# Kernel tuning notes

Hardware: AMD Instinct MI355X
Metric: run time of the kernel (lower is better)

## Reference

```python
import jax, jax.numpy as jnp
import numpy as np

GN_EPS = 1e-5
G = 8          # SKA groups
SKS3 = 27      # sks**3


def _aff(x, s, b):
    # folded BatchNorm (eval): per-channel scale + shift on NCDHW tensor
    return x * s[None, :, None, None, None] + b[None, :, None, None, None]


def _c1(x, w):
    # 1x1x1 conv as channel GEMM; w: [O, I]
    return jnp.einsum('bcdhw,oc->bodhw', x, w)


def _dw5(x, w):
    # depthwise 5x5x5 conv, pad=2; w: [C, 1, 5, 5, 5]
    return jax.lax.conv_general_dilated(
        x, w, window_strides=(1, 1, 1), padding=[(2, 2)] * 3,
        dimension_numbers=('NCDHW', 'OIDHW', 'NCDHW'),
        feature_group_count=x.shape[1])


def setup_inputs() -> dict:
    key = jax.random.key(0)
    ks = jax.random.split(key, 24)
    B, C, D, H, W = 2, 64, 32, 32, 32

    def n(k, shape, scale=1.0):
        return jax.random.normal(k, shape, jnp.float32) * scale

    def u(k, shape):
        return jax.random.uniform(k, shape, jnp.float32, 0.5, 1.5)

    return {
        'x': n(ks[0], (B, C, D, H, W)),
        'w1': n(ks[1], (32, 64), 64 ** -0.5),
        's1': u(ks[2], (32,)), 'b1': n(ks[3], (32,), 0.1),
        'w2': n(ks[4], (32, 1, 5, 5, 5), 125 ** -0.5),
        's2': u(ks[5], (32,)), 'b2': n(ks[6], (32,), 0.1),
        'w3': n(ks[7], (32, 32), 32 ** -0.5),
        's3': u(ks[8], (32,)), 'b3': n(ks[9], (32,), 0.1),
        'w4': n(ks[10], (216, 32), 32 ** -0.5), 'b4': n(ks[11], (216,), 0.1),
        'gn_g': u(ks[12], (216,)), 'gn_b': n(ks[13], (216,), 0.1),
        'bn_s': u(ks[14], (64,)), 'bn_b': n(ks[15], (64,), 0.1),
        'pw1_w': n(ks[16], (128, 64), 64 ** -0.5),
        'pw1_s': u(ks[17], (128,)), 'pw1_b': n(ks[18], (128,), 0.1),
        'pw2_w': n(ks[19], (64, 128), 128 ** -0.5),
        'pw2_s': u(ks[20], (64,)), 'pw2_b': n(ks[21], (64,), 0.1),
    }


def reference(x, w1, s1, b1, w2, s2, b2, w3, s3, b3, w4, b4,
              gn_g, gn_b, bn_s, bn_b,
              pw1_w, pw1_s, pw1_b, pw2_w, pw2_s, pw2_b):
    B, C, D, H, W = x.shape

    # ---- LKP3D: dynamic kernel generation ----
    a = jax.nn.relu(_aff(_c1(x, w1), s1, b1))          # cv1 + BN + ReLU
    a = _aff(_dw5(a, w2), s2, b2)                      # cv2 (5^3 dw) + BN
    a = jax.nn.relu(_aff(_c1(a, w3), s3, b3))          # cv3 + BN + ReLU
    wk = _c1(a, w4) + b4[None, :, None, None, None]    # cv4: [B,216,D,H,W]
    # GroupNorm: num_groups = dim//groups = 8, channels = 216
    g = wk.reshape(B, G, SKS3, D, H, W)
    mu = g.mean(axis=(2, 3, 4, 5), keepdims=True)
    var = g.var(axis=(2, 3, 4, 5), keepdims=True)
    g = (g - mu) * jax.lax.rsqrt(var + GN_EPS)
    wk = g.reshape(B, G * SKS3, D, H, W) * gn_g[None, :, None, None, None] \
         + gn_b[None, :, None, None, None]
    wk = wk.reshape(B, G, SKS3, D, H, W)               # [B, G, 27, D, H, W]

    # ---- SKA3D: apply dynamic kernels (27 shifted copies, grouped) ----
    offs = [(di, hi, wi) for di in (-1, 0, 1) for hi in (-1, 0, 1) for wi in (-1, 0, 1)]
    patches = jnp.stack(
        [jnp.roll(x, (-di, -hi, -wi), axis=(2, 3, 4)) for di, hi, wi in offs],
        axis=2)                                        # [B, C, 27, D, H, W]
    p = patches.reshape(B, G, C // G, SKS3, D, H, W)
    sk = jnp.einsum('bgckdhw,bgkdhw->bgcdhw', p, wk).reshape(B, C, D, H, W)

    y = _aff(sk, bn_s, bn_b) + x                       # LSConv BN + residual

    # ---- FFN (residual): pw1 + BN + ReLU + pw2 + BN ----
    f = jax.nn.relu(_aff(_c1(y, pw1_w), pw1_s, pw1_b))
    f = _aff(_c1(f, pw2_w), pw2_s, pw2_b)
    return y + f
```

## Files before the change

### kernel.cpp

```cpp
#include <hip/hip_runtime.h>
#include <hip/hip_bf16.h>

#define SPAT 32768
#define BATCH 2
#define GN_EPS 1e-5f

__device__ __forceinline__ void fma4(float4& a, const float4& v, float w) {
    a.x = fmaf(v.x, w, a.x); a.y = fmaf(v.y, w, a.y);
    a.z = fmaf(v.z, w, a.z); a.w = fmaf(v.w, w, a.w);
}

template <bool RELU, bool AFF>
__global__ __launch_bounds__(256) void k_c1(
    const float* __restrict__ in, const float* __restrict__ w,
    const float* __restrict__ sc, const float* __restrict__ bi,
    float* __restrict__ out, int Cin, int Cout)
{
    int q = blockIdx.x * 256 + threadIdx.x;
    int s = q * 4;
    int o0 = blockIdx.y * 4, b = blockIdx.z;
    const float* ip = in + (size_t)b * Cin * SPAT + s;
    float4 a0 = {0,0,0,0}, a1 = a0, a2 = a0, a3 = a0;
#pragma unroll 4
    for (int c = 0; c < Cin; ++c) {
        float4 v = *(const float4*)(ip + (size_t)c * SPAT);
        fma4(a0, v, w[(o0+0)*Cin + c]);
        fma4(a1, v, w[(o0+1)*Cin + c]);
        fma4(a2, v, w[(o0+2)*Cin + c]);
        fma4(a3, v, w[(o0+3)*Cin + c]);
    }
    float4 accs[4] = {a0, a1, a2, a3};
#pragma unroll
    for (int i = 0; i < 4; ++i) {
        int o = o0 + i;
        float scale = AFF ? sc[o] : 1.f;
        float shift = bi[o];
        float4 r = accs[i];
        r.x = r.x * scale + shift; r.y = r.y * scale + shift;
        r.z = r.z * scale + shift; r.w = r.w * scale + shift;
        if (RELU) {
            r.x = fmaxf(r.x, 0.f); r.y = fmaxf(r.y, 0.f);
            r.z = fmaxf(r.z, 0.f); r.w = fmaxf(r.w, 0.f);
        }
        *(float4*)(out + ((size_t)b * Cout + o) * SPAT + s) = r;
    }
}

__global__ __launch_bounds__(256) void k_dw5(
    const float* __restrict__ in, const float* __restrict__ w2,
    const float* __restrict__ s2, const float* __restrict__ b2,
    float* __restrict__ out)
{
    __shared__ float lds[8 * 36 * 40];
    int tid = threadIdx.x;
    int d0 = blockIdx.x * 4;
    int c = blockIdx.y, b = blockIdx.z;
    const float* ip = in + ((size_t)(b * 32 + c)) * SPAT;

    float4 z = {0,0,0,0};
    for (int i = tid; i < 8 * 36 * 40 / 4; i += 256)
        ((float4*)lds)[i] = z;
    __syncthreads();
    for (int i = tid; i < 8 * 256; i += 256) {
        int p = i >> 8, rem = i & 255;
        int r = rem >> 3, c4 = (rem & 7) * 4;
        int d = d0 - 2 + p;
        if (d >= 0 && d < 32) {
            float4 v = *(const float4*)(ip + d * 1024 + r * 32 + c4);
            *(float4*)&lds[p * 1440 + (r + 2) * 40 + (c4 + 4)] = v;
        }
    }
    __syncthreads();

    float scl = s2[c], shf = b2[c];
    const float* wt = w2 + c * 125;
#pragma unroll
    for (int k = 0; k < 4; ++k) {
        int j = tid + k * 256;
        int pd = j >> 8, rem = j & 255;
        int hr = rem >> 3, w4 = (rem & 7) * 4;
        float4 acc = {0,0,0,0};
#pragma unroll
        for (int kd = 0; kd < 5; ++kd) {
            const float* pl = &lds[(pd + kd) * 1440];
#pragma unroll
            for (int kh = 0; kh < 5; ++kh) {
                const float* row = pl + (hr + kh) * 40 + w4;
                float4 r0 = *(const float4*)(row);
                float4 r1 = *(const float4*)(row + 4);
                float4 r2 = *(const float4*)(row + 8);
                float win[12] = {r0.x, r0.y, r0.z, r0.w,
                                 r1.x, r1.y, r1.z, r1.w,
                                 r2.x, r2.y, r2.z, r2.w};
#pragma unroll
                for (int kw = 0; kw < 5; ++kw) {
                    float wv = wt[kd * 25 + kh * 5 + kw];
                    acc.x = fmaf(wv, win[2 + 0 + kw], acc.x);
                    acc.y = fmaf(wv, win[2 + 1 + kw], acc.y);
                    acc.z = fmaf(wv, win[2 + 2 + kw], acc.z);
                    acc.w = fmaf(wv, win[2 + 3 + kw], acc.w);
                }
            }
        }
        acc.x = acc.x * scl + shf; acc.y = acc.y * scl + shf;
        acc.z = acc.z * scl + shf; acc.w = acc.w * scl + shf;
        *(float4*)(out + ((size_t)(b * 32 + c)) * SPAT
                   + (d0 + pd) * 1024 + hr * 32 + w4) = acc;
    }
}

__global__ __launch_bounds__(256) void k_gn_part(
    const float* __restrict__ wk, float* __restrict__ partial)
{
    int bg = blockIdx.y;
    const float4* p = (const float4*)(wk + (size_t)bg * 27 * SPAT
                                      + (size_t)blockIdx.x * 16384);
    float sum = 0.f, ss = 0.f;
    for (int i = threadIdx.x; i < 4096; i += 256) {
        float4 v = p[i];
        sum += v.x + v.y + v.z + v.w;
        ss += v.x*v.x + v.y*v.y + v.z*v.z + v.w*v.w;
    }
    __shared__ float sh[512];
    sh[threadIdx.x] = sum; sh[256 + threadIdx.x] = ss;
    __syncthreads();
    for (int off = 128; off > 0; off >>= 1) {
        if (threadIdx.x < off) {
            sh[threadIdx.x] += sh[threadIdx.x + off];
            sh[256 + threadIdx.x] += sh[256 + threadIdx.x + off];
        }
        __syncthreads();
    }
    if (threadIdx.x == 0) {
        partial[(bg * 54 + blockIdx.x) * 2 + 0] = sh[0];
        partial[(bg * 54 + blockIdx.x) * 2 + 1] = sh[256];
    }
}

__global__ void k_gn_final(const float* __restrict__ partial, float* __restrict__ stats)
{
    int bg = blockIdx.x;
    int t = threadIdx.x;
    float sum = 0.f, ss = 0.f;
    if (t < 54) {
        sum = partial[(bg * 54 + t) * 2 + 0];
        ss  = partial[(bg * 54 + t) * 2 + 1];
    }
#pragma unroll
    for (int off = 32; off > 0; off >>= 1) {
        sum += __shfl_down(sum, off, 64);
        ss  += __shfl_down(ss,  off, 64);
    }
    if (t == 0) {
        stats[bg * 2 + 0] = sum;
        stats[bg * 2 + 1] = ss;
    }
}

__global__ __launch_bounds__(256) void k_ska(
    const float* __restrict__ x, const float* __restrict__ wk,
    const float* __restrict__ stats,
    const float* __restrict__ gn_g, const float* __restrict__ gn_b,
    const float* __restrict__ bn_s, const float* __restrict__ bn_b,
    float* __restrict__ y)
{
    int q = blockIdx.x * 256 + threadIdx.x;
    int s = q * 4;
    int g = blockIdx.y, b = blockIdx.z;
    int bg = b * 8 + g;
    const float N = 27.f * (float)SPAT;
    float mu  = stats[bg * 2 + 0] / N;
    float var = stats[bg * 2 + 1] / N - mu * mu;
    float inv = rsqrtf(var + GN_EPS);
    int d = s >> 10, h = (s >> 5) & 31, w0 = s & 31;
    const float* xg = x + ((size_t)(b * 64 + g * 8)) * SPAT;
    const float* wp = wk + ((size_t)(b * 216 + g * 27)) * SPAT + s;

    float4 acc[8];
#pragma unroll
    for (int c = 0; c < 8; ++c) acc[c] = {0,0,0,0};

#pragma unroll
    for (int kd = 0; kd < 3; ++kd) {
        int zd = (d + kd + 31) & 31;
#pragma unroll
        for (int kh = 0; kh < 3; ++kh) {
            int zh = (h + kh + 31) & 31;
            int kbase = (kd * 3 + kh) * 3;
            float wn[3][4];
#pragma unroll
            for (int kw = 0; kw < 3; ++kw) {
                int kk = kbase + kw;
                float4 wq = *(const float4*)(wp + (size_t)kk * SPAT);
                float gg = gn_g[g * 27 + kk], gb = gn_b[g * 27 + kk];
                wn[kw][0] = (wq.x - mu) * inv * gg + gb;
                wn[kw][1] = (wq.y - mu) * inv * gg + gb;
                wn[kw][2] = (wq.z - mu) * inv * gg + gb;
                wn[kw][3] = (wq.w - mu) * inv * gg + gb;
            }
            int rowoff = zd * 1024 + zh * 32;
#pragma unroll
            for (int c = 0; c < 8; ++c) {
                const float* row = xg + (size_t)c * SPAT + rowoff;
                float4 m = *(const float4*)(row + w0);
                float xl = row[(w0 + 31) & 31];
                float xr = row[(w0 + 4) & 31];
                float win[6] = {xl, m.x, m.y, m.z, m.w, xr};
#pragma unroll
                for (int kw = 0; kw < 3; ++kw) {
                    acc[c].x = fmaf(win[0 + kw], wn[kw][0], acc[c].x);
                    acc[c].y = fmaf(win[1 + kw], wn[kw][1], acc[c].y);
                    acc[c].z = fmaf(win[2 + kw], wn[kw][2], acc[c].z);
                    acc[c].w = fmaf(win[3 + kw], wn[kw][3], acc[c].w);
                }
            }
        }
    }
#pragma unroll
    for (int c = 0; c < 8; ++c) {
        int ch = g * 8 + c;
        float4 xc = *(const float4*)(xg + (size_t)c * SPAT + s);
        float bs = bn_s[ch], bb = bn_b[ch];
        float4 r;
        r.x = acc[c].x * bs + bb + xc.x;
        r.y = acc[c].y * bs + bb + xc.y;
        r.z = acc[c].z * bs + bb + xc.z;
        r.w = acc[c].w * bs + bb + xc.w;
        *(float4*)(y + ((size_t)(b * 64 + ch)) * SPAT + s) = r;
    }
}

__global__ __launch_bounds__(256) void k_pw2_out(
    const float* __restrict__ f1, const float* __restrict__ w,
    const float* __restrict__ sc, const float* __restrict__ bi,
    const float* __restrict__ yres, float* __restrict__ out)
{
    int q = blockIdx.x * 256 + threadIdx.x;
    int s = q * 4;
    int o0 = blockIdx.y * 4, b = blockIdx.z;
    const float* ip = f1 + (size_t)b * 128 * SPAT + s;
    float4 a0 = {0,0,0,0}, a1 = a0, a2 = a0, a3 = a0;
#pragma unroll 4
    for (int c = 0; c < 128; ++c) {
        float4 v = *(const float4*)(ip + (size_t)c * SPAT);
        fma4(a0, v, w[(o0+0)*128 + c]);
        fma4(a1, v, w[(o0+1)*128 + c]);
        fma4(a2, v, w[(o0+2)*128 + c]);
        fma4(a3, v, w[(o0+3)*128 + c]);
    }
    float4 accs[4] = {a0, a1, a2, a3};
#pragma unroll
    for (int i = 0; i < 4; ++i) {
        int o = o0 + i;
        float scale = sc[o], shift = bi[o];
        float4 yv = *(const float4*)(yres + ((size_t)(b * 64 + o)) * SPAT + s);
        float4 r = accs[i];
        r.x = r.x * scale + shift + yv.x;
        r.y = r.y * scale + shift + yv.y;
        r.z = r.z * scale + shift + yv.z;
        r.w = r.w * scale + shift + yv.w;
        *(float4*)(out + ((size_t)(b * 64 + o)) * SPAT + s) = r;
    }
}

extern "C" void kernel_launch(void* const* d_in, const int* in_sizes, int n_in,
                              void* d_out, int out_size, void* d_ws, size_t ws_size,
                              hipStream_t stream)
{
    const float* x     = (const float*)d_in[0];
    const float* w1    = (const float*)d_in[1];
    const float* s1    = (const float*)d_in[2];
    const float* b1    = (const float*)d_in[3];
    const float* w2    = (const float*)d_in[4];
    const float* s2    = (const float*)d_in[5];
    const float* b2    = (const float*)d_in[6];
    const float* w3    = (const float*)d_in[7];
    const float* s3    = (const float*)d_in[8];
    const float* b3    = (const float*)d_in[9];
    const float* w4    = (const float*)d_in[10];
    const float* b4    = (const float*)d_in[11];
    const float* gn_g  = (const float*)d_in[12];
    const float* gn_b  = (const float*)d_in[13];
    const float* bn_s  = (const float*)d_in[14];
    const float* bn_b  = (const float*)d_in[15];
    const float* pw1_w = (const float*)d_in[16];
    const float* pw1_s = (const float*)d_in[17];
    const float* pw1_b = (const float*)d_in[18];
    const float* pw2_w = (const float*)d_in[19];
    const float* pw2_s = (const float*)d_in[20];
    const float* pw2_b = (const float*)d_in[21];

    float* ws    = (float*)d_ws;
    float* a1    = ws;
    float* a2    = a1 + (size_t)BATCH * 32 * SPAT;
    float* yb    = ws;
    float* wkb   = ws + (size_t)BATCH * 64 * SPAT;
    float* f1    = wkb;
    float* part  = wkb + (size_t)BATCH * 216 * SPAT;
    float* stats = part + 16 * 54 * 2;

    dim3 blk(256);
    k_c1<true, true><<<dim3(SPAT / 1024, 8, BATCH), blk, 0, stream>>>(
        x, w1, s1, b1, a1, 64, 32);
    k_dw5<<<dim3(8, 32, BATCH), blk, 0, stream>>>(a1, w2, s2, b2, a2);
    k_c1<true, true><<<dim3(SPAT / 1024, 8, BATCH), blk, 0, stream>>>(
        a2, w3, s3, b3, a1, 32, 32);
    k_c1<false, false><<<dim3(SPAT / 1024, 54, BATCH), blk, 0, stream>>>(
        a1, w4, (const float*)nullptr, b4, wkb, 32, 216);
    k_gn_part<<<dim3(54, 16, 1), blk, 0, stream>>>(wkb, part);
    k_gn_final<<<dim3(16, 1, 1), dim3(64), 0, stream>>>(part, stats);
    k_ska<<<dim3(SPAT / 1024, 8, BATCH), blk, 0, stream>>>(
        x, wkb, stats, gn_g, gn_b, bn_s, bn_b, yb);
    k_c1<true, true><<<dim3(SPAT / 1024, 32, BATCH), blk, 0, stream>>>(
        yb, pw1_w, pw1_s, pw1_b, f1, 64, 128);
    k_pw2_out<<<dim3(SPAT / 1024, 16, BATCH), blk, 0, stream>>>(
        f1, pw2_w, pw2_s, pw2_b, yb, (float*)d_out);
}
```

Before: 250.0 us.

## Fuse GroupNorm statistics into cv4 GEMM and use lane shuffles in SKA

The cv4 pointwise conv kernel now computes per-block sum and sum-of-squares partials while writing its output. This removes the separate GN partial pass, which reread the whole 216-channel wk tensor, and a tiny kernel now reduces those partials. The SKA kernel gets its left and right W-neighbours through wave shuffles instead of scalar global loads, and keeps the center x values in registers for the residual so they are not reloaded. This adds reduction work and register pressure to cv4 and SKA. The shuffle wrap logic relies on 8 lanes covering exactly one 32-wide row.

```diff
diff --git a/kernel.cpp b/kernel.cpp
--- a/kernel.cpp
+++ b/kernel.cpp
@@ -46,6 +46,171 @@
     }
 }
 
+__global__ __launch_bounds__(256) void k_cv4(
+    const float* __restrict__ in, const float* __restrict__ w,
+    const float* __restrict__ bi, float* __restrict__ out,
+    float* __restrict__ partial)
+{
+    int q = blockIdx.x * 256 + threadIdx.x;
+    int s = q * 4;
+    int o0 = blockIdx.y * 4, b = blockIdx.z;
+    const float* ip = in + (size_t)b * 32 * SPAT + s;
+    float4 a0 = {0,0,0,0}, a1 = a0, a2 = a0, a3 = a0;
+#pragma unroll 4
+    for (int c = 0; c < 32; ++c) {
+        float4 v = *(const float4*)(ip + (size_t)c * SPAT);
+        fma4(a0, v, w[(o0+0)*32 + c]);
+        fma4(a1, v, w[(o0+1)*32 + c]);
+        fma4(a2, v, w[(o0+2)*32 + c]);
+        fma4(a3, v, w[(o0+3)*32 + c]);
+    }
+    float4 accs[4] = {a0, a1, a2, a3};
+    float sums[4], sss[4];
+#pragma unroll
+    for (int i = 0; i < 4; ++i) {
+        int o = o0 + i;
+        float shift = bi[o];
+        float4 r = accs[i];
+        r.x += shift; r.y += shift; r.z += shift; r.w += shift;
+        *(float4*)(out + ((size_t)b * 216 + o) * SPAT + s) = r;
+        sums[i] = r.x + r.y + r.z + r.w;
+        sss[i]  = r.x*r.x + r.y*r.y + r.z*r.z + r.w*r.w;
+    }
+#pragma unroll
+    for (int off = 32; off > 0; off >>= 1) {
+#pragma unroll
+        for (int i = 0; i < 4; ++i) {
+            sums[i] += __shfl_down(sums[i], off, 64);
+            sss[i]  += __shfl_down(sss[i],  off, 64);
+        }
+    }
+    __shared__ float sh[4][4][2];
+    int wave = threadIdx.x >> 6, lane = threadIdx.x & 63;
+    if (lane == 0) {
+#pragma unroll
+        for (int i = 0; i < 4; ++i) {
+            sh[wave][i][0] = sums[i];
+            sh[wave][i][1] = sss[i];
+        }
+    }
+    __syncthreads();
+    if (threadIdx.x < 4) {
+        int i = threadIdx.x;
+        float s0 = sh[0][i][0] + sh[1][i][0] + sh[2][i][0] + sh[3][i][0];
+        float s1 = sh[0][i][1] + sh[1][i][1] + sh[2][i][1] + sh[3][i][1];
+        int o = o0 + i;
+        int idx = (((b * 216 + o) * 32) + blockIdx.x) * 2;
+        partial[idx + 0] = s0;
+        partial[idx + 1] = s1;
+    }
+}
+
+__global__ __launch_bounds__(256) void k_gn_stats2(
+    const float* __restrict__ partial, float* __restrict__ stats)
+{
+    int bg = blockIdx.x;
+    int b = bg >> 3, g = bg & 7;
+    float sum = 0.f, ss = 0.f;
+    for (int i = threadIdx.x; i < 27 * 32; i += 256) {
+        int o = g * 27 + (i >> 5);
+        int xb = i & 31;
+        int idx = ((b * 216 + o) * 32 + xb) * 2;
+        sum += partial[idx + 0];
+        ss  += partial[idx + 1];
+    }
+    __shared__ float sh[512];
+    sh[threadIdx.x] = sum; sh[256 + threadIdx.x] = ss;
+    __syncthreads();
+    for (int off = 128; off > 0; off >>= 1) {
+        if (threadIdx.x < off) {
+            sh[threadIdx.x] += sh[threadIdx.x + off];
+            sh[256 + threadIdx.x] += sh[256 + threadIdx.x + off];
+        }
+        __syncthreads();
+    }
+    if (threadIdx.x == 0) {
+        stats[bg * 2 + 0] = sh[0];
+        stats[bg * 2 + 1] = sh[256];
+    }
+}
+
+__global__ __launch_bounds__(256) void k_ska(
+    const float* __restrict__ x, const float* __restrict__ wk,
+    const float* __restrict__ stats,
+    const float* __restrict__ gn_g, const float* __restrict__ gn_b,
+    const float* __restrict__ bn_s, const float* __restrict__ bn_b,
+    float* __restrict__ y)
+{
+    int q = blockIdx.x * 256 + threadIdx.x;
+    int s = q * 4;
+    int g = blockIdx.y, b = blockIdx.z;
+    int bg = b * 8 + g;
+    const float N = 27.f * (float)SPAT;
+    float mu  = stats[bg * 2 + 0] / N;
+    float var = stats[bg * 2 + 1] / N - mu * mu;
+    float inv = rsqrtf(var + GN_EPS);
+    int d = s >> 10, h = (s >> 5) & 31, w0 = s & 31;
+    int lane = threadIdx.x & 63;
+    int xl_src = (lane & 56) | ((lane + 7) & 7);
+    int xr_src = (lane & 56) | ((lane + 1) & 7);
+    const float* xg = x + ((size_t)(b * 64 + g * 8)) * SPAT;
+    const float* wp = wk + ((size_t)(b * 216 + g * 27)) * SPAT + s;
+
+    float4 acc[8];
+    float4 xc[8];
+#pragma unroll
+    for (int c = 0; c < 8; ++c) acc[c] = {0,0,0,0};
+
+#pragma unroll
+    for (int kd = 0; kd < 3; ++kd) {
+        int zd = (d + kd + 31) & 31;
+#pragma unroll
+        for (int kh = 0; kh < 3; ++kh) {
+            int zh = (h + kh + 31) & 31;
+            int kbase = (kd * 3 + kh) * 3;
+            float wn[3][4];
+#pragma unroll
+            for (int kw = 0; kw < 3; ++kw) {
+                int kk = kbase + kw;
+                float4 wq = *(const float4*)(wp + (size_t)kk * SPAT);
+                float gg = gn_g[g * 27 + kk], gb = gn_b[g * 27 + kk];
+                wn[kw][0] = (wq.x - mu) * inv * gg + gb;
+                wn[kw][1] = (wq.y - mu) * inv * gg + gb;
+                wn[kw][2] = (wq.z - mu) * inv * gg + gb;
+                wn[kw][3] = (wq.w - mu) * inv * gg + gb;
+            }
+            int rowoff = zd * 1024 + zh * 32;
+            bool center = (kd == 1) && (kh == 1);
+#pragma unroll
+            for (int c = 0; c < 8; ++c) {
+                float4 m = *(const float4*)(xg + (size_t)c * SPAT + rowoff + w0);
+                if (center) xc[c] = m;
+                float xl = __shfl(m.w, xl_src, 64);
+                float xr = __shfl(m.x, xr_src, 64);
+                float win[6] = {xl, m.x, m.y, m.z, m.w, xr};
+#pragma unroll
+                for (int kw = 0; kw < 3; ++kw) {
+                    acc[c].x = fmaf(win[0 + kw], wn[kw][0], acc[c].x);
+                    acc[c].y = fmaf(win[1 + kw], wn[kw][1], acc[c].y);
+                    acc[c].z = fmaf(win[2 + kw], wn[kw][2], acc[c].z);
+                    acc[c].w = fmaf(win[3 + kw], wn[kw][3], acc[c].w);
+                }
+            }
+        }
+    }
+#pragma unroll
+    for (int c = 0; c < 8; ++c) {
+        int ch = g * 8 + c;
+        float bs = bn_s[ch], bb = bn_b[ch];
+        float4 r;
+        r.x = acc[c].x * bs + bb + xc[c].x;
+        r.y = acc[c].y * bs + bb + xc[c].y;
+        r.z = acc[c].z * bs + bb + xc[c].z;
+        r.w = acc[c].w * bs + bb + xc[c].w;
+        *(float4*)(y + ((size_t)(b * 64 + ch)) * SPAT + s) = r;
+    }
+}
+
 __global__ __launch_bounds__(256) void k_dw5(
     const float* __restrict__ in, const float* __restrict__ w2,
     const float* __restrict__ s2, const float* __restrict__ b2,
@@ -106,127 +271,6 @@
         acc.z = acc.z * scl + shf; acc.w = acc.w * scl + shf;
         *(float4*)(out + ((size_t)(b * 32 + c)) * SPAT
                    + (d0 + pd) * 1024 + hr * 32 + w4) = acc;
-    }
-}
-
-__global__ __launch_bounds__(256) void k_gn_part(
-    const float* __restrict__ wk, float* __restrict__ partial)
-{
-    int bg = blockIdx.y;
-    const float4* p = (const float4*)(wk + (size_t)bg * 27 * SPAT
-                                      + (size_t)blockIdx.x * 16384);
-    float sum = 0.f, ss = 0.f;
-    for (int i = threadIdx.x; i < 4096; i += 256) {
-        float4 v = p[i];
-        sum += v.x + v.y + v.z + v.w;
-        ss += v.x*v.x + v.y*v.y + v.z*v.z + v.w*v.w;
-    }
-    __shared__ float sh[512];
-    sh[threadIdx.x] = sum; sh[256 + threadIdx.x] = ss;
-    __syncthreads();
-    for (int off = 128; off > 0; off >>= 1) {
-        if (threadIdx.x < off) {
-            sh[threadIdx.x] += sh[threadIdx.x + off];
-            sh[256 + threadIdx.x] += sh[256 + threadIdx.x + off];
-        }
-        __syncthreads();
-    }
-    if (threadIdx.x == 0) {
-        partial[(bg * 54 + blockIdx.x) * 2 + 0] = sh[0];
-        partial[(bg * 54 + blockIdx.x) * 2 + 1] = sh[256];
-    }
-}
-
-__global__ void k_gn_final(const float* __restrict__ partial, float* __restrict__ stats)
-{
-    int bg = blockIdx.x;
-    int t = threadIdx.x;
-    float sum = 0.f, ss = 0.f;
-    if (t < 54) {
-        sum = partial[(bg * 54 + t) * 2 + 0];
-        ss  = partial[(bg * 54 + t) * 2 + 1];
-    }
-#pragma unroll
-    for (int off = 32; off > 0; off >>= 1) {
-        sum += __shfl_down(sum, off, 64);
-        ss  += __shfl_down(ss,  off, 64);
-    }
-    if (t == 0) {
-        stats[bg * 2 + 0] = sum;
-        stats[bg * 2 + 1] = ss;
-    }
-}
-
-__global__ __launch_bounds__(256) void k_ska(
-    const float* __restrict__ x, const float* __restrict__ wk,
-    const float* __restrict__ stats,
-    const float* __restrict__ gn_g, const float* __restrict__ gn_b,
-    const float* __restrict__ bn_s, const float* __restrict__ bn_b,
-    float* __restrict__ y)
-{
-    int q = blockIdx.x * 256 + threadIdx.x;
-    int s = q * 4;
-    int g = blockIdx.y, b = blockIdx.z;
-    int bg = b * 8 + g;
-    const float N = 27.f * (float)SPAT;
-    float mu  = stats[bg * 2 + 0] / N;
-    float var = stats[bg * 2 + 1] / N - mu * mu;
-    float inv = rsqrtf(var + GN_EPS);
-    int d = s >> 10, h = (s >> 5) & 31, w0 = s & 31;
-    const float* xg = x + ((size_t)(b * 64 + g * 8)) * SPAT;
-    const float* wp = wk + ((size_t)(b * 216 + g * 27)) * SPAT + s;
-
-    float4 acc[8];
-#pragma unroll
-    for (int c = 0; c < 8; ++c) acc[c] = {0,0,0,0};
-
-#pragma unroll
-    for (int kd = 0; kd < 3; ++kd) {
-        int zd = (d + kd + 31) & 31;
-#pragma unroll
-        for (int kh = 0; kh < 3; ++kh) {
-            int zh = (h + kh + 31) & 31;
-            int kbase = (kd * 3 + kh) * 3;
-            float wn[3][4];
-#pragma unroll
-            for (int kw = 0; kw < 3; ++kw) {
-                int kk = kbase + kw;
-                float4 wq = *(const float4*)(wp + (size_t)kk * SPAT);
-                float gg = gn_g[g * 27 + kk], gb = gn_b[g * 27 + kk];
-                wn[kw][0] = (wq.x - mu) * inv * gg + gb;
-                wn[kw][1] = (wq.y - mu) * inv * gg + gb;
-                wn[kw][2] = (wq.z - mu) * inv * gg + gb;
-                wn[kw][3] = (wq.w - mu) * inv * gg + gb;
-            }
-            int rowoff = zd * 1024 + zh * 32;
-#pragma unroll
-            for (int c = 0; c < 8; ++c) {
-                const float* row = xg + (size_t)c * SPAT + rowoff;
-                float4 m = *(const float4*)(row + w0);
-                float xl = row[(w0 + 31) & 31];
-                float xr = row[(w0 + 4) & 31];
-                float win[6] = {xl, m.x, m.y, m.z, m.w, xr};
-#pragma unroll
-                for (int kw = 0; kw < 3; ++kw) {
-                    acc[c].x = fmaf(win[0 + kw], wn[kw][0], acc[c].x);
-                    acc[c].y = fmaf(win[1 + kw], wn[kw][1], acc[c].y);
-                    acc[c].z = fmaf(win[2 + kw], wn[kw][2], acc[c].z);
-                    acc[c].w = fmaf(win[3 + kw], wn[kw][3], acc[c].w);
-                }
-            }
-        }
-    }
-#pragma unroll
-    for (int c = 0; c < 8; ++c) {
-        int ch = g * 8 + c;
-        float4 xc = *(const float4*)(xg + (size_t)c * SPAT + s);
-        float bs = bn_s[ch], bb = bn_b[ch];
-        float4 r;
-        r.x = acc[c].x * bs + bb + xc.x;
-        r.y = acc[c].y * bs + bb + xc.y;
-        r.z = acc[c].z * bs + bb + xc.z;
-        r.w = acc[c].w * bs + bb + xc.w;
-        *(float4*)(y + ((size_t)(b * 64 + ch)) * SPAT + s) = r;
     }
 }
 
@@ -297,7 +341,7 @@
     float* wkb   = ws + (size_t)BATCH * 64 * SPAT;
     float* f1    = wkb;
     float* part  = wkb + (size_t)BATCH * 216 * SPAT;
-    float* stats = part + 16 * 54 * 2;
+    float* stats = part + BATCH * 216 * 32 * 2;
 
     dim3 blk(256);
     k_c1<true, true><<<dim3(SPAT / 1024, 8, BATCH), blk, 0, stream>>>(
@@ -305,10 +349,9 @@
     k_dw5<<<dim3(8, 32, BATCH), blk, 0, stream>>>(a1, w2, s2, b2, a2);
     k_c1<true, true><<<dim3(SPAT / 1024, 8, BATCH), blk, 0, stream>>>(
         a2, w3, s3, b3, a1, 32, 32);
-    k_c1<false, false><<<dim3(SPAT / 1024, 54, BATCH), blk, 0, stream>>>(
-        a1, w4, (const float*)nullptr, b4, wkb, 32, 216);
-    k_gn_part<<<dim3(54, 16, 1), blk, 0, stream>>>(wkb, part);
-    k_gn_final<<<dim3(16, 1, 1), dim3(64), 0, stream>>>(part, stats);
+    k_cv4<<<dim3(SPAT / 1024, 54, BATCH), blk, 0, stream>>>(
+        a1, w4, b4, wkb, part);
+    k_gn_stats2<<<dim3(16, 1, 1), blk, 0, stream>>>(part, stats);
     k_ska<<<dim3(SPAT / 1024, 8, BATCH), blk, 0, stream>>>(
         x, wkb, stats, gn_g, gn_b, bn_s, bn_b, yb);
     k_c1<true, true><<<dim3(SPAT / 1024, 32, BATCH), blk, 0, stream>>>(
```

New measurement: 231.4 us. 1.08x faster.
